# Performance work log

Measured on AMD Instinct MI355X. Metric: run time of the kernel, lower is better.

The kernel has to match this reference:

```python
import jax, jax.numpy as jnp
import numpy as np

B, C = 2048, 512          # batch, channels
CHG = 16                  # coarse grid side (16x16 -> N=256)
FHG = 16                  # fine grid side (16x16 -> F=256)
N = CHG * CHG             # coarse_span.total
F = FHG * FHG             # fine_total
K = 4                     # top4 sample mode
LOG_F = float(np.log(F))


def _ln(x, g, b, eps=1e-5):
    m = jnp.mean(x, axis=-1, keepdims=True)
    v = jnp.var(x, axis=-1, keepdims=True)
    return (x - m) * jax.lax.rsqrt(v + eps) * g + b


def _mlp3(x, w1, b1, w2, b2, w3, b3):
    # linear_stack: Linear+gelu, Linear+gelu, Linear (dropout=0 / eval)
    h = jax.nn.gelu(x @ w1 + b1)
    h = jax.nn.gelu(h @ w2 + b2)
    return h @ w3 + b3


def setup_inputs() -> dict:
    key = jax.random.key(0)
    ks = jax.random.split(key, 10)
    s = 0.02
    return {
        'x': jax.random.normal(ks[0], (B, C), jnp.float32),
        'in_g': jnp.ones((C,), jnp.float32), 'in_b': jnp.zeros((C,), jnp.float32),
        'nop_w': jax.random.normal(ks[1], (C, 1), jnp.float32) * s,
        'nop_b': jnp.zeros((1,), jnp.float32),
        'c_w1': jax.random.normal(ks[2], (C, C), jnp.float32) * s,
        'c_b1': jnp.zeros((C,), jnp.float32),
        'c_w2': jax.random.normal(ks[3], (C, C), jnp.float32) * s,
        'c_b2': jnp.zeros((C,), jnp.float32),
        'c_w3': jax.random.normal(ks[4], (C, N), jnp.float32) * s,
        'c_b3': jnp.zeros((N,), jnp.float32),
        'emb': jax.random.normal(ks[5], (N, C), jnp.float32),
        'emb_g': jnp.ones((C,), jnp.float32), 'emb_b': jnp.zeros((C,), jnp.float32),
        'f_w1': jax.random.normal(ks[6], (2 * C, C), jnp.float32) * s,
        'f_b1': jnp.zeros((C,), jnp.float32),
        'f_w2': jax.random.normal(ks[7], (C, C), jnp.float32) * s,
        'f_b2': jnp.zeros((C,), jnp.float32),
        'f_w3': jax.random.normal(ks[8], (C, F), jnp.float32) * s,
        'f_b3': jnp.zeros((F,), jnp.float32),
    }


def reference(x, in_g, in_b, nop_w, nop_b, c_w1, c_b1, c_w2, c_b2, c_w3, c_b3,
              emb, emb_g, emb_b, f_w1, f_b1, f_w2, f_b2, f_w3, f_b3):
    xn = _ln(x, in_g, in_b)                                  # (B,C)
    no_op = xn @ nop_w + nop_b                               # (B,1)
    coarse = _mlp3(xn, c_w1, c_b1, c_w2, c_b2, c_w3, c_b3)   # (B,N)
    _, idx = jax.lax.top_k(coarse, K)                        # (B,K) int32
    e = _ln(emb[idx], emb_g, emb_b)                          # (B,K,C)
    fin = jnp.concatenate([jnp.broadcast_to(xn[:, None, :], (B, K, C)), e], axis=-1)
    fine = _mlp3(fin, f_w1, f_b1, f_w2, f_b2, f_w3, f_b3)    # (B,K,F)
    # scatter value: coarse[b,i] - log F + fine + log F - lse(fine) = coarse[b,i] + log_softmax(fine)
    vals = jnp.take_along_axis(coarse, idx, axis=1)[:, :, None] + jax.nn.log_softmax(fine, axis=-1)
    dense = jnp.broadcast_to((coarse - LOG_F)[:, :, None], (B, N, F))
    dense = dense.at[jnp.arange(B)[:, None], idx].set(vals)  # top-k indices are distinct
    # view (B, ch0, ch1, fh0, fh1) -> permute (0,1,3,2,4) -> flatten
    xname = dense.reshape(B, CHG, CHG, FHG, FHG).transpose(0, 1, 3, 2, 4).reshape(B, -1)
    return jnp.concatenate([no_op, xname], axis=-1)          # (B, 1 + N*F)
```

## Files before the change

kernel.cpp:

```cpp
#include <hip/hip_runtime.h>
#include <math.h>

#define BATCH 2048
#define CH 512
#define N_COARSE 256
#define F_FINE 256
#define K_TOP 4
#define OUT_STRIDE 65537

typedef unsigned short ushort_t;
typedef __bf16 bf16x8 __attribute__((ext_vector_type(8)));
typedef float f32x4 __attribute__((ext_vector_type(4)));

__device__ __forceinline__ float gelu_tanh(float x) {
    float x3 = x * x * x;
    float t = tanhf(0.7978845608028654f * (x + 0.044715f * x3));
    return 0.5f * x * (1.0f + t);
}

__device__ __forceinline__ ushort_t f2bf(float f) {
    unsigned u = __float_as_uint(f);
    unsigned r = (u + 0x7FFF + ((u >> 16) & 1)) >> 16;
    return (ushort_t)r;
}
__device__ __forceinline__ float bf2f(ushort_t h) {
    return __uint_as_float(((unsigned)h) << 16);
}

__global__ __launch_bounds__(256) void prep_kernel(
    const float* __restrict__ f_w1, const float* __restrict__ f_w2, const float* __restrict__ f_w3,
    ushort_t* __restrict__ wt1, ushort_t* __restrict__ wt2, ushort_t* __restrict__ wt3,
    const float* __restrict__ c_w1, const float* __restrict__ c_w2, const float* __restrict__ c_w3,
    ushort_t* __restrict__ cwt1, ushort_t* __restrict__ cwt2, ushort_t* __restrict__ cwt3,
    const float* __restrict__ x, const float* __restrict__ g, const float* __restrict__ b,
    const float* __restrict__ nop_w, const float* __restrict__ nop_b,
    ushort_t* __restrict__ xnsp, float* __restrict__ out)
{
    __shared__ float s[32][33];
    int blk = blockIdx.x;
    int t = threadIdx.x;
    if (blk < 1536) {
        const float* W; ushort_t* Wt; int Kd, Nd, gx, gy; bool split;
        if (blk < 512)       { W=f_w1; Wt=wt1; Kd=1024; Nd=512; gx=blk&15; gy=blk>>4; split=false; }
        else if (blk < 768)  { int u=blk-512;  W=f_w2; Wt=wt2; Kd=512; Nd=512; gx=u&15; gy=u>>4; split=false; }
        else if (blk < 896)  { int u=blk-768;  W=f_w3; Wt=wt3; Kd=512; Nd=256; gx=u&7;  gy=u>>3; split=false; }
        else if (blk < 1152) { int u=blk-896;  W=c_w1; Wt=cwt1; Kd=512; Nd=512; gx=u&15; gy=u>>4; split=true; }
        else if (blk < 1408) { int u=blk-1152; W=c_w2; Wt=cwt2; Kd=512; Nd=512; gx=u&15; gy=u>>4; split=true; }
        else                 { int u=blk-1408; W=c_w3; Wt=cwt3; Kd=512; Nd=256; gx=u&7;  gy=u>>3; split=true; }
        int tx = t & 31, ty = t >> 5;
        int n0 = gx * 32, k0 = gy * 32;
        #pragma unroll
        for (int i = 0; i < 4; ++i) {
            int r = ty + i * 8;
            s[r][tx] = W[(size_t)(k0 + r) * Nd + n0 + tx];
        }
        __syncthreads();
        if (!split) {
            #pragma unroll
            for (int i = 0; i < 4; ++i) {
                int r = ty + i * 8;
                Wt[(size_t)(n0 + r) * Kd + k0 + tx] = f2bf(s[tx][r]);
            }
        } else {
            #pragma unroll
            for (int i = 0; i < 4; ++i) {
                int r = ty + i * 8;
                float v = s[tx][r];
                ushort_t h = f2bf(v);
                Wt[(size_t)(n0 + r) * 1024 + k0 + tx] = h;
                Wt[(size_t)(n0 + r) * 1024 + 512 + k0 + tx] = f2bf(v - bf2f(h));
            }
        }
    } else {
        float* red = &s[0][0];
        int row = blk - 1536;
        int lane = t & 63, wave = t >> 6;
        const float* xr = x + (size_t)row * CH;
        float v0 = xr[t], v1 = xr[t + 256];
        float sm = v0 + v1, ss = v0 * v0 + v1 * v1;
        #pragma unroll
        for (int off = 32; off; off >>= 1) { sm += __shfl_xor(sm, off); ss += __shfl_xor(ss, off); }
        if (lane == 0) { red[wave] = sm; red[4 + wave] = ss; }
        __syncthreads();
        sm = red[0] + red[1] + red[2] + red[3];
        ss = red[4] + red[5] + red[6] + red[7];
        float mean = sm * (1.0f / CH);
        float var = ss * (1.0f / CH) - mean * mean;
        float rsq = rsqrtf(var + 1e-5f);
        float xn0 = (v0 - mean) * rsq * g[t] + b[t];
        float xn1 = (v1 - mean) * rsq * g[t + 256] + b[t + 256];
        ushort_t* xr2 = xnsp + (size_t)row * 1024;
        ushort_t h0 = f2bf(xn0), h1v = f2bf(xn1);
        xr2[t] = h0; xr2[t + 256] = h1v;
        xr2[512 + t] = f2bf(xn0 - bf2f(h0));
        xr2[512 + t + 256] = f2bf(xn1 - bf2f(h1v));
        float d = xn0 * nop_w[t] + xn1 * nop_w[t + 256];
        #pragma unroll
        for (int off = 32; off; off >>= 1) d += __shfl_xor(d, off);
        __syncthreads();
        if (lane == 0) red[wave] = d;
        __syncthreads();
        if (t == 0) out[(size_t)row * OUT_STRIDE] = red[0] + red[1] + red[2] + red[3] + nop_b[0];
    }
}

template<int MODE, int MT, int NT, int OUTM>
__global__ __launch_bounds__(256) void mfma_gemm_kernel(
    const ushort_t* __restrict__ A1, const ushort_t* __restrict__ A2,
    const ushort_t* __restrict__ Wt, const float* __restrict__ bias,
    const float* __restrict__ cvals, void* __restrict__ Cout, int Nd, int Ktot)
{
    constexpr int AI = MT / 64, BI = NT / 64;
    constexpr int FI = MT / 32, FJ = NT / 32;
    __shared__ ushort_t As[2][MT * 32];
    __shared__ ushort_t Bs[2][NT * 32];
    __shared__ float mxs[64 * 2];
    __shared__ float ses[64 * 2];
    int t = threadIdx.x;
    int n0 = blockIdx.x * NT, m0 = blockIdx.y * MT;
    int wave = t >> 6, lane = t & 63;
    int wm = (wave & 1) * (MT / 2), wn = (wave >> 1) * (NT / 2);
    int lr = lane & 15, quad = lane >> 4;

    f32x4 acc[FI][FJ] = {};
    float4 aReg[AI], bReg[BI];

    auto loadAB = [&](int k0) {
        int aoff = (MODE == 2) ? ((k0 >= 1024) ? k0 - 512 : (k0 & 511)) : k0;
        int woff = (MODE == 2) ? ((k0 >= 1024) ? k0 - 1024 : k0) : k0;
        #pragma unroll
        for (int i = 0; i < AI; ++i) {
            int c = i * 256 + t, r = c >> 2, q = (c & 3) * 8;
            int gr = m0 + r;
            const ushort_t* ap;
            if (MODE == 1)      ap = (k0 < 512) ? A1 + (size_t)(gr >> 2) * 1024 + k0 + q
                                                : A2 + (size_t)gr * 512 + (k0 - 512) + q;
            else if (MODE == 2) ap = A1 + (size_t)gr * 1024 + aoff + q;
            else                ap = A1 + (size_t)gr * Ktot + k0 + q;
            aReg[i] = *(const float4*)ap;
        }
        #pragma unroll
        for (int i = 0; i < BI; ++i) {
            int c = i * 256 + t, r = c >> 2, q = (c & 3) * 8;
            size_t wstride = (MODE == 2) ? 1024 : (size_t)Ktot;
            bReg[i] = *(const float4*)(Wt + (size_t)(n0 + r) * wstride + woff + q);
        }
    };
    auto storeAB = [&](int p) {
        #pragma unroll
        for (int i = 0; i < AI; ++i) { int c = i * 256 + t; *(float4*)&As[p][c * 8] = aReg[i]; }
        #pragma unroll
        for (int i = 0; i < BI; ++i) { int c = i * 256 + t; *(float4*)&Bs[p][c * 8] = bReg[i]; }
    };

    loadAB(0);
    storeAB(0);
    int steps = Ktot >> 5;
    int p = 0;
    for (int s = 0; s < steps; ++s) {
        __syncthreads();
        if (s + 1 < steps) loadAB((s + 1) * 32);
        bf16x8 af[FI], bfr[FJ];
        #pragma unroll
        for (int i = 0; i < FI; ++i)
            af[i] = *(const bf16x8*)&As[p][(wm + i * 16 + lr) * 32 + quad * 8];
        #pragma unroll
        for (int j = 0; j < FJ; ++j)
            bfr[j] = *(const bf16x8*)&Bs[p][(wn + j * 16 + lr) * 32 + quad * 8];
        #pragma unroll
        for (int i = 0; i < FI; ++i)
            #pragma unroll
            for (int j = 0; j < FJ; ++j)
                acc[i][j] = __builtin_amdgcn_mfma_f32_16x16x32_bf16(af[i], bfr[j], acc[i][j], 0, 0, 0);
        if (s + 1 < steps) storeAB(p ^ 1);
        p ^= 1;
    }

    if (OUTM == 3) {
        float bv[FJ];
        #pragma unroll
        for (int j = 0; j < FJ; ++j) bv[j] = bias[wn + j * 16 + lr];
        int half = wave >> 1;
        float rmx[FI][4];
        #pragma unroll
        for (int i = 0; i < FI; ++i)
            #pragma unroll
            for (int r = 0; r < 4; ++r) {
                float m = -1e30f;
                #pragma unroll
                for (int j = 0; j < FJ; ++j) m = fmaxf(m, acc[i][j][r] + bv[j]);
                #pragma unroll
                for (int mk = 1; mk < 16; mk <<= 1) m = fmaxf(m, __shfl_xor(m, mk));
                if (lr == 0) mxs[(wm + i * 16 + quad * 4 + r) * 2 + half] = m;
            }
        __syncthreads();
        #pragma unroll
        for (int i = 0; i < FI; ++i)
            #pragma unroll
            for (int r = 0; r < 4; ++r) {
                int rl = wm + i * 16 + quad * 4 + r;
                rmx[i][r] = fmaxf(mxs[rl * 2], mxs[rl * 2 + 1]);
            }
        #pragma unroll
        for (int i = 0; i < FI; ++i)
            #pragma unroll
            for (int r = 0; r < 4; ++r) {
                float sv = 0.f;
                #pragma unroll
                for (int j = 0; j < FJ; ++j) sv += expf(acc[i][j][r] + bv[j] - rmx[i][r]);
                #pragma unroll
                for (int mk = 1; mk < 16; mk <<= 1) sv += __shfl_xor(sv, mk);
                if (lr == 0) ses[(wm + i * 16 + quad * 4 + r) * 2 + half] = sv;
            }
        __syncthreads();
        float* outp = (float*)Cout;
        #pragma unroll
        for (int i = 0; i < FI; ++i)
            #pragma unroll
            for (int r = 0; r < 4; ++r) {
                int rl = wm + i * 16 + quad * 4 + r;
                float se = ses[rl * 2] + ses[rl * 2 + 1];
                float addc = cvals[m0 + rl] - rmx[i][r] - logf(se);
                #pragma unroll
                for (int j = 0; j < FJ; ++j)
                    outp[(size_t)(m0 + rl) * Nd + wn + j * 16 + lr] = acc[i][j][r] + bv[j] + addc;
            }
    } else {
        #pragma unroll
        for (int j = 0; j < FJ; ++j) {
            int col = n0 + wn + j * 16 + lr;
            float bvv = bias[col];
            #pragma unroll
            for (int i = 0; i < FI; ++i) {
                #pragma unroll
                for (int r = 0; r < 4; ++r) {
                    int row = m0 + wm + i * 16 + quad * 4 + r;
                    float val = acc[i][j][r] + bvv;
                    if (OUTM == 0) {
                        ((ushort_t*)Cout)[(size_t)row * Nd + col] = f2bf(gelu_tanh(val));
                    } else if (OUTM == 1) {
                        float gv = gelu_tanh(val);
                        ushort_t h = f2bf(gv);
                        ((ushort_t*)Cout)[(size_t)row * 1024 + col] = h;
                        ((ushort_t*)Cout)[(size_t)row * 1024 + 512 + col] = f2bf(gv - bf2f(h));
                    } else {
                        ((float*)Cout)[(size_t)row * Nd + col] = val;
                    }
                }
            }
        }
    }
}

__global__ __launch_bounds__(256) void topk_embln_kernel(
    const float* __restrict__ coarse, const float* __restrict__ emb,
    const float* __restrict__ g, const float* __restrict__ b,
    int* __restrict__ idx, float* __restrict__ cvals, ushort_t* __restrict__ e_bf)
{
    int brow = blockIdx.x;
    int t = threadIdx.x;
    int wave = t >> 6, lane = t & 63;
    __shared__ int sidx[4];

    if (wave == 0) {
        const float* cr = coarse + (size_t)brow * N_COARSE;
        float v[4]; int id[4];
        #pragma unroll
        for (int j = 0; j < 4; ++j) { v[j] = cr[lane + 64 * j]; id[j] = lane + 64 * j; }
        #pragma unroll
        for (int r = 0; r < K_TOP; ++r) {
            float bv = v[0]; int bi = id[0];
            #pragma unroll
            for (int j = 1; j < 4; ++j)
                if (v[j] > bv || (v[j] == bv && id[j] < bi)) { bv = v[j]; bi = id[j]; }
            #pragma unroll
            for (int off = 32; off; off >>= 1) {
                float ov = __shfl_xor(bv, off); int oi = __shfl_xor(bi, off);
                if (ov > bv || (ov == bv && oi < bi)) { bv = ov; bi = oi; }
            }
            if ((bi & 63) == lane) v[bi >> 6] = -INFINITY;
            if (lane == 0) {
                sidx[r] = bi;
                idx[brow * K_TOP + r] = bi;
                cvals[brow * K_TOP + r] = bv;
            }
        }
    }
    __syncthreads();

    int n = sidx[wave];
    const float* er = emb + (size_t)n * CH + lane * 8;
    float4 u0 = *(const float4*)er;
    float4 u1 = *(const float4*)(er + 4);
    float s  = u0.x + u0.y + u0.z + u0.w + u1.x + u1.y + u1.z + u1.w;
    float ss = u0.x * u0.x + u0.y * u0.y + u0.z * u0.z + u0.w * u0.w
             + u1.x * u1.x + u1.y * u1.y + u1.z * u1.z + u1.w * u1.w;
    #pragma unroll
    for (int off = 32; off; off >>= 1) { s += __shfl_xor(s, off); ss += __shfl_xor(ss, off); }
    float mean = s * (1.0f / CH);
    float var = ss * (1.0f / CH) - mean * mean;
    float rsq = rsqrtf(var + 1e-5f);
    float4 g0 = *(const float4*)(g + lane * 8), g1 = *(const float4*)(g + lane * 8 + 4);
    float4 b0 = *(const float4*)(b + lane * 8), b1 = *(const float4*)(b + lane * 8 + 4);
    uint4 pk;
    pk.x = (unsigned)f2bf((u0.x - mean) * rsq * g0.x + b0.x) |
           ((unsigned)f2bf((u0.y - mean) * rsq * g0.y + b0.y) << 16);
    pk.y = (unsigned)f2bf((u0.z - mean) * rsq * g0.z + b0.z) |
           ((unsigned)f2bf((u0.w - mean) * rsq * g0.w + b0.w) << 16);
    pk.z = (unsigned)f2bf((u1.x - mean) * rsq * g1.x + b1.x) |
           ((unsigned)f2bf((u1.y - mean) * rsq * g1.y + b1.y) << 16);
    pk.w = (unsigned)f2bf((u1.z - mean) * rsq * g1.z + b1.z) |
           ((unsigned)f2bf((u1.w - mean) * rsq * g1.w + b1.w) << 16);
    *(uint4*)(e_bf + (size_t)(brow * K_TOP + wave) * CH + lane * 8) = pk;
}

__global__ __launch_bounds__(256) void scatter_kernel(
    const float* __restrict__ coarse, const float* __restrict__ fine,
    const int* __restrict__ idx, float* __restrict__ out)
{
    const float LOG_F = 5.545177444479562f;
    int b = blockIdx.y;
    __shared__ int sidx[4];
    if (threadIdx.x < 4) sidx[threadIdx.x] = idx[b * 4 + threadIdx.x];
    __syncthreads();
    int i0 = sidx[0], i1 = sidx[1], i2 = sidx[2], i3 = sidx[3];
    size_t rowb = (size_t)b * OUT_STRIDE + 1;
    #pragma unroll
    for (int q = 0; q < 4; ++q) {
        int o = blockIdx.x * 4096 + q * 1024 + threadIdx.x * 4;
        int c0 = o >> 12, f0 = (o >> 8) & 15, c1 = (o >> 4) & 15, f1 = o & 15;
        int n = c0 * 16 + c1;
        int f = f0 * 16 + f1;
        int k = -1;
        if (n == i0) k = 0; else if (n == i1) k = 1; else if (n == i2) k = 2; else if (n == i3) k = 3;
        float r0, r1, r2, r3;
        if (k >= 0) {
            float4 u = *(const float4*)(fine + ((size_t)(b * 4 + k)) * F_FINE + f);
            r0 = u.x; r1 = u.y; r2 = u.z; r3 = u.w;
        } else {
            float base = coarse[(size_t)b * N_COARSE + n] - LOG_F;
            r0 = r1 = r2 = r3 = base;
        }
        float* p = out + rowb + o;
        __builtin_nontemporal_store(r0, p + 0);
        __builtin_nontemporal_store(r1, p + 1);
        __builtin_nontemporal_store(r2, p + 2);
        __builtin_nontemporal_store(r3, p + 3);
    }
}

extern "C" void kernel_launch(void* const* d_in, const int* in_sizes, int n_in,
                              void* d_out, int out_size, void* d_ws, size_t ws_size,
                              hipStream_t stream) {
    const float* x     = (const float*)d_in[0];
    const float* in_g  = (const float*)d_in[1];
    const float* in_b  = (const float*)d_in[2];
    const float* nop_w = (const float*)d_in[3];
    const float* nop_b = (const float*)d_in[4];
    const float* c_w1  = (const float*)d_in[5];
    const float* c_b1  = (const float*)d_in[6];
    const float* c_w2  = (const float*)d_in[7];
    const float* c_b2  = (const float*)d_in[8];
    const float* c_w3  = (const float*)d_in[9];
    const float* c_b3  = (const float*)d_in[10];
    const float* emb   = (const float*)d_in[11];
    const float* emb_g = (const float*)d_in[12];
    const float* emb_b = (const float*)d_in[13];
    const float* f_w1  = (const float*)d_in[14];
    const float* f_b1  = (const float*)d_in[15];
    const float* f_w2  = (const float*)d_in[16];
    const float* f_b2  = (const float*)d_in[17];
    const float* f_w3  = (const float*)d_in[18];
    const float* f_b3  = (const float*)d_in[19];

    float* ws = (float*)d_ws;
    float* coarse  = ws;
    float* fine    = coarse + 524288;
    ushort_t* xnsp   = (ushort_t*)(fine + 2097152);
    ushort_t* h1sp   = xnsp + 2097152;
    ushort_t* h2sp   = h1sp + 2097152;
    ushort_t* e_bf   = h2sp + 2097152;
    ushort_t* fh1_bf = e_bf + 4194304;
    ushort_t* fh2_bf = fh1_bf + 4194304;
    ushort_t* wt1    = fh2_bf + 4194304;
    ushort_t* wt2    = wt1 + 524288;
    ushort_t* wt3    = wt2 + 262144;
    ushort_t* cwt1   = wt3 + 131072;
    ushort_t* cwt2   = cwt1 + 524288;
    ushort_t* cwt3   = cwt2 + 524288;
    int*   idxb   = (int*)(cwt3 + 262144);
    float* cvals  = (float*)(idxb + 8192);

    float* out = (float*)d_out;

    prep_kernel<<<3584, 256, 0, stream>>>(
        f_w1, f_w2, f_w3, wt1, wt2, wt3,
        c_w1, c_w2, c_w3, cwt1, cwt2, cwt3,
        x, in_g, in_b, nop_w, nop_b, xnsp, out);
    mfma_gemm_kernel<2, 64, 64, 1><<<dim3(8, 32), 256, 0, stream>>>(
        xnsp, nullptr, cwt1, c_b1, nullptr, h1sp, 512, 1536);
    mfma_gemm_kernel<2, 64, 64, 1><<<dim3(8, 32), 256, 0, stream>>>(
        h1sp, nullptr, cwt2, c_b2, nullptr, h2sp, 512, 1536);
    mfma_gemm_kernel<2, 64, 64, 2><<<dim3(4, 32), 256, 0, stream>>>(
        h2sp, nullptr, cwt3, c_b3, nullptr, coarse, 256, 1536);
    topk_embln_kernel<<<BATCH, 256, 0, stream>>>(coarse, emb, emb_g, emb_b, idxb, cvals, e_bf);
    mfma_gemm_kernel<1, 64, 128, 0><<<dim3(4, 128), 256, 0, stream>>>(
        xnsp, e_bf, wt1, f_b1, nullptr, fh1_bf, 512, 1024);
    mfma_gemm_kernel<0, 64, 128, 0><<<dim3(4, 128), 256, 0, stream>>>(
        fh1_bf, nullptr, wt2, f_b2, nullptr, fh2_bf, 512, 512);
    mfma_gemm_kernel<0, 64, 256, 3><<<dim3(1, 128), 256, 0, stream>>>(
        fh2_bf, nullptr, wt3, f_b3, cvals, fine, 256, 512);
    scatter_kernel<<<dim3(16, BATCH), 256, 0, stream>>>(coarse, fine, idxb, out);
}
```

Baseline: 760.2 us.

## Fuse all stages into one persistent cooperative kernel with grid syncs

Replaces the sequence of nine kernel launches with a single cooperative persistent kernel of 256 blocks that runs each stage in a loop over work units and separates stages with grid-wide barriers. The fine-MLP GEMMs use larger 128x128 tiles to fit the fixed grid. This targets launch gaps and tail effects between small stages, but limits the bandwidth-bound scatter and other stages to one block per CU, which may reduce memory-level parallelism. A fallback to the original multi-kernel path is kept if the cooperative launch fails.

```diff
diff --git a/kernel.cpp b/kernel.cpp
--- a/kernel.cpp
+++ b/kernel.cpp
@@ -1,5 +1,8 @@
 #include <hip/hip_runtime.h>
+#include <hip/hip_cooperative_groups.h>
 #include <math.h>
+
+namespace cg = cooperative_groups;
 
 #define BATCH 2048
 #define CH 512
@@ -27,26 +30,27 @@
     return __uint_as_float(((unsigned)h) << 16);
 }
 
-__global__ __launch_bounds__(256) void prep_kernel(
-    const float* __restrict__ f_w1, const float* __restrict__ f_w2, const float* __restrict__ f_w3,
-    ushort_t* __restrict__ wt1, ushort_t* __restrict__ wt2, ushort_t* __restrict__ wt3,
-    const float* __restrict__ c_w1, const float* __restrict__ c_w2, const float* __restrict__ c_w3,
-    ushort_t* __restrict__ cwt1, ushort_t* __restrict__ cwt2, ushort_t* __restrict__ cwt3,
-    const float* __restrict__ x, const float* __restrict__ g, const float* __restrict__ b,
-    const float* __restrict__ nop_w, const float* __restrict__ nop_b,
-    ushort_t* __restrict__ xnsp, float* __restrict__ out)
-{
-    __shared__ float s[32][33];
-    int blk = blockIdx.x;
-    int t = threadIdx.x;
-    if (blk < 1536) {
+struct Params {
+    const float *x, *in_g, *in_b, *nop_w, *nop_b;
+    const float *c_w1, *c_b1, *c_w2, *c_b2, *c_w3, *c_b3;
+    const float *emb, *emb_g, *emb_b;
+    const float *f_w1, *f_b1, *f_w2, *f_b2, *f_w3, *f_b3;
+    float *coarse, *fine, *out, *cvals;
+    ushort_t *xnsp, *h1sp, *h2sp, *e_bf, *fh1_bf, *fh2_bf;
+    ushort_t *wt1, *wt2, *wt3, *cwt1, *cwt2, *cwt3;
+    int *idxb;
+};
+
+__device__ __forceinline__ void prep_unit(char* smem, int u, int t, const Params& p) {
+    if (u < 1536) {
+        float (*s)[33] = (float(*)[33])smem;
         const float* W; ushort_t* Wt; int Kd, Nd, gx, gy; bool split;
-        if (blk < 512)       { W=f_w1; Wt=wt1; Kd=1024; Nd=512; gx=blk&15; gy=blk>>4; split=false; }
-        else if (blk < 768)  { int u=blk-512;  W=f_w2; Wt=wt2; Kd=512; Nd=512; gx=u&15; gy=u>>4; split=false; }
-        else if (blk < 896)  { int u=blk-768;  W=f_w3; Wt=wt3; Kd=512; Nd=256; gx=u&7;  gy=u>>3; split=false; }
-        else if (blk < 1152) { int u=blk-896;  W=c_w1; Wt=cwt1; Kd=512; Nd=512; gx=u&15; gy=u>>4; split=true; }
-        else if (blk < 1408) { int u=blk-1152; W=c_w2; Wt=cwt2; Kd=512; Nd=512; gx=u&15; gy=u>>4; split=true; }
-        else                 { int u=blk-1408; W=c_w3; Wt=cwt3; Kd=512; Nd=256; gx=u&7;  gy=u>>3; split=true; }
+        if (u < 512)       { W=p.f_w1; Wt=p.wt1; Kd=1024; Nd=512; gx=u&15; gy=u>>4; split=false; }
+        else if (u < 768)  { int v=u-512;  W=p.f_w2; Wt=p.wt2; Kd=512; Nd=512; gx=v&15; gy=v>>4; split=false; }
+        else if (u < 896)  { int v=u-768;  W=p.f_w3; Wt=p.wt3; Kd=512; Nd=256; gx=v&7;  gy=v>>3; split=false; }
+        else if (u < 1152) { int v=u-896;  W=p.c_w1; Wt=p.cwt1; Kd=512; Nd=512; gx=v&15; gy=v>>4; split=true; }
+        else if (u < 1408) { int v=u-1152; W=p.c_w2; Wt=p.cwt2; Kd=512; Nd=512; gx=v&15; gy=v>>4; split=true; }
+        else               { int v=u-1408; W=p.c_w3; Wt=p.cwt3; Kd=512; Nd=256; gx=v&7;  gy=v>>3; split=true; }
         int tx = t & 31, ty = t >> 5;
         int n0 = gx * 32, k0 = gy * 32;
         #pragma unroll
@@ -72,10 +76,10 @@
             }
         }
     } else {
-        float* red = &s[0][0];
-        int row = blk - 1536;
+        float* red = (float*)smem;
+        int row = u - 1536;
         int lane = t & 63, wave = t >> 6;
-        const float* xr = x + (size_t)row * CH;
+        const float* xr = p.x + (size_t)row * CH;
         float v0 = xr[t], v1 = xr[t + 256];
         float sm = v0 + v1, ss = v0 * v0 + v1 * v1;
         #pragma unroll
@@ -87,37 +91,36 @@
         float mean = sm * (1.0f / CH);
         float var = ss * (1.0f / CH) - mean * mean;
         float rsq = rsqrtf(var + 1e-5f);
-        float xn0 = (v0 - mean) * rsq * g[t] + b[t];
-        float xn1 = (v1 - mean) * rsq * g[t + 256] + b[t + 256];
-        ushort_t* xr2 = xnsp + (size_t)row * 1024;
+        float xn0 = (v0 - mean) * rsq * p.in_g[t] + p.in_b[t];
+        float xn1 = (v1 - mean) * rsq * p.in_g[t + 256] + p.in_b[t + 256];
+        ushort_t* xr2 = p.xnsp + (size_t)row * 1024;
         ushort_t h0 = f2bf(xn0), h1v = f2bf(xn1);
         xr2[t] = h0; xr2[t + 256] = h1v;
         xr2[512 + t] = f2bf(xn0 - bf2f(h0));
         xr2[512 + t + 256] = f2bf(xn1 - bf2f(h1v));
-        float d = xn0 * nop_w[t] + xn1 * nop_w[t + 256];
+        float d = xn0 * p.nop_w[t] + xn1 * p.nop_w[t + 256];
         #pragma unroll
         for (int off = 32; off; off >>= 1) d += __shfl_xor(d, off);
         __syncthreads();
         if (lane == 0) red[wave] = d;
         __syncthreads();
-        if (t == 0) out[(size_t)row * OUT_STRIDE] = red[0] + red[1] + red[2] + red[3] + nop_b[0];
+        if (t == 0) p.out[(size_t)row * OUT_STRIDE] = red[0] + red[1] + red[2] + red[3] + p.nop_b[0];
     }
 }
 
 template<int MODE, int MT, int NT, int OUTM>
-__global__ __launch_bounds__(256) void mfma_gemm_kernel(
+__device__ __forceinline__ void mfma_tile(
+    char* smem, int t, int n0, int m0,
     const ushort_t* __restrict__ A1, const ushort_t* __restrict__ A2,
     const ushort_t* __restrict__ Wt, const float* __restrict__ bias,
     const float* __restrict__ cvals, void* __restrict__ Cout, int Nd, int Ktot)
 {
     constexpr int AI = MT / 64, BI = NT / 64;
     constexpr int FI = MT / 32, FJ = NT / 32;
-    __shared__ ushort_t As[2][MT * 32];
-    __shared__ ushort_t Bs[2][NT * 32];
-    __shared__ float mxs[64 * 2];
-    __shared__ float ses[64 * 2];
-    int t = threadIdx.x;
-    int n0 = blockIdx.x * NT, m0 = blockIdx.y * MT;
+    ushort_t* As = (ushort_t*)smem;
+    ushort_t* Bs = (ushort_t*)(smem + MT * 128);
+    float* mxs = (float*)(smem + (MT + NT) * 128);
+    float* ses = mxs + 128;
     int wave = t >> 6, lane = t & 63;
     int wm = (wave & 1) * (MT / 2), wn = (wave >> 1) * (NT / 2);
     int lr = lane & 15, quad = lane >> 4;
@@ -148,9 +151,9 @@
     };
     auto storeAB = [&](int p) {
         #pragma unroll
-        for (int i = 0; i < AI; ++i) { int c = i * 256 + t; *(float4*)&As[p][c * 8] = aReg[i]; }
-        #pragma unroll
-        for (int i = 0; i < BI; ++i) { int c = i * 256 + t; *(float4*)&Bs[p][c * 8] = bReg[i]; }
+        for (int i = 0; i < AI; ++i) { int c = i * 256 + t; *(float4*)&As[p * MT * 32 + c * 8] = aReg[i]; }
+        #pragma unroll
+        for (int i = 0; i < BI; ++i) { int c = i * 256 + t; *(float4*)&Bs[p * NT * 32 + c * 8] = bReg[i]; }
     };
 
     loadAB(0);
@@ -163,10 +166,10 @@
         bf16x8 af[FI], bfr[FJ];
         #pragma unroll
         for (int i = 0; i < FI; ++i)
-            af[i] = *(const bf16x8*)&As[p][(wm + i * 16 + lr) * 32 + quad * 8];
+            af[i] = *(const bf16x8*)&As[p * MT * 32 + (wm + i * 16 + lr) * 32 + quad * 8];
         #pragma unroll
         for (int j = 0; j < FJ; ++j)
-            bfr[j] = *(const bf16x8*)&Bs[p][(wn + j * 16 + lr) * 32 + quad * 8];
+            bfr[j] = *(const bf16x8*)&Bs[p * NT * 32 + (wn + j * 16 + lr) * 32 + quad * 8];
         #pragma unroll
         for (int i = 0; i < FI; ++i)
             #pragma unroll
@@ -252,18 +255,11 @@
     }
 }
 
-__global__ __launch_bounds__(256) void topk_embln_kernel(
-    const float* __restrict__ coarse, const float* __restrict__ emb,
-    const float* __restrict__ g, const float* __restrict__ b,
-    int* __restrict__ idx, float* __restrict__ cvals, ushort_t* __restrict__ e_bf)
-{
-    int brow = blockIdx.x;
-    int t = threadIdx.x;
+__device__ __forceinline__ void topk_embln_block(char* smem, int brow, int t, const Params& p) {
     int wave = t >> 6, lane = t & 63;
-    __shared__ int sidx[4];
-
+    int* sidx = (int*)smem;
     if (wave == 0) {
-        const float* cr = coarse + (size_t)brow * N_COARSE;
+        const float* cr = p.coarse + (size_t)brow * N_COARSE;
         float v[4]; int id[4];
         #pragma unroll
         for (int j = 0; j < 4; ++j) { v[j] = cr[lane + 64 * j]; id[j] = lane + 64 * j; }
@@ -281,15 +277,14 @@
             if ((bi & 63) == lane) v[bi >> 6] = -INFINITY;
             if (lane == 0) {
                 sidx[r] = bi;
-                idx[brow * K_TOP + r] = bi;
-                cvals[brow * K_TOP + r] = bv;
+                p.idxb[brow * K_TOP + r] = bi;
+                p.cvals[brow * K_TOP + r] = bv;
             }
         }
     }
     __syncthreads();
-
     int n = sidx[wave];
-    const float* er = emb + (size_t)n * CH + lane * 8;
+    const float* er = p.emb + (size_t)n * CH + lane * 8;
     float4 u0 = *(const float4*)er;
     float4 u1 = *(const float4*)(er + 4);
     float s  = u0.x + u0.y + u0.z + u0.w + u1.x + u1.y + u1.z + u1.w;
@@ -300,8 +295,8 @@
     float mean = s * (1.0f / CH);
     float var = ss * (1.0f / CH) - mean * mean;
     float rsq = rsqrtf(var + 1e-5f);
-    float4 g0 = *(const float4*)(g + lane * 8), g1 = *(const float4*)(g + lane * 8 + 4);
-    float4 b0 = *(const float4*)(b + lane * 8), b1 = *(const float4*)(b + lane * 8 + 4);
+    float4 g0 = *(const float4*)(p.emb_g + lane * 8), g1 = *(const float4*)(p.emb_g + lane * 8 + 4);
+    float4 b0 = *(const float4*)(p.emb_b + lane * 8), b1 = *(const float4*)(p.emb_b + lane * 8 + 4);
     uint4 pk;
     pk.x = (unsigned)f2bf((u0.x - mean) * rsq * g0.x + b0.x) |
            ((unsigned)f2bf((u0.y - mean) * rsq * g0.y + b0.y) << 16);
@@ -311,104 +306,158 @@
            ((unsigned)f2bf((u1.y - mean) * rsq * g1.y + b1.y) << 16);
     pk.w = (unsigned)f2bf((u1.z - mean) * rsq * g1.z + b1.z) |
            ((unsigned)f2bf((u1.w - mean) * rsq * g1.w + b1.w) << 16);
-    *(uint4*)(e_bf + (size_t)(brow * K_TOP + wave) * CH + lane * 8) = pk;
-}
-
-__global__ __launch_bounds__(256) void scatter_kernel(
-    const float* __restrict__ coarse, const float* __restrict__ fine,
-    const int* __restrict__ idx, float* __restrict__ out)
-{
+    *(uint4*)(p.e_bf + (size_t)(brow * K_TOP + wave) * CH + lane * 8) = pk;
+}
+
+__device__ __forceinline__ void scatter_unit(int b, int cx, int t, const Params& p) {
     const float LOG_F = 5.545177444479562f;
-    int b = blockIdx.y;
-    __shared__ int sidx[4];
-    if (threadIdx.x < 4) sidx[threadIdx.x] = idx[b * 4 + threadIdx.x];
-    __syncthreads();
-    int i0 = sidx[0], i1 = sidx[1], i2 = sidx[2], i3 = sidx[3];
+    int4 ii = *(const int4*)&p.idxb[b * 4];
     size_t rowb = (size_t)b * OUT_STRIDE + 1;
     #pragma unroll
     for (int q = 0; q < 4; ++q) {
-        int o = blockIdx.x * 4096 + q * 1024 + threadIdx.x * 4;
+        int o = cx * 4096 + q * 1024 + t * 4;
         int c0 = o >> 12, f0 = (o >> 8) & 15, c1 = (o >> 4) & 15, f1 = o & 15;
         int n = c0 * 16 + c1;
         int f = f0 * 16 + f1;
         int k = -1;
-        if (n == i0) k = 0; else if (n == i1) k = 1; else if (n == i2) k = 2; else if (n == i3) k = 3;
+        if (n == ii.x) k = 0; else if (n == ii.y) k = 1; else if (n == ii.z) k = 2; else if (n == ii.w) k = 3;
         float r0, r1, r2, r3;
         if (k >= 0) {
-            float4 u = *(const float4*)(fine + ((size_t)(b * 4 + k)) * F_FINE + f);
+            float4 u = *(const float4*)(p.fine + ((size_t)(b * 4 + k)) * F_FINE + f);
             r0 = u.x; r1 = u.y; r2 = u.z; r3 = u.w;
         } else {
-            float base = coarse[(size_t)b * N_COARSE + n] - LOG_F;
+            float base = p.coarse[(size_t)b * N_COARSE + n] - LOG_F;
             r0 = r1 = r2 = r3 = base;
         }
-        float* p = out + rowb + o;
-        __builtin_nontemporal_store(r0, p + 0);
-        __builtin_nontemporal_store(r1, p + 1);
-        __builtin_nontemporal_store(r2, p + 2);
-        __builtin_nontemporal_store(r3, p + 3);
-    }
+        float* op = p.out + rowb + o;
+        __builtin_nontemporal_store(r0, op + 0);
+        __builtin_nontemporal_store(r1, op + 1);
+        __builtin_nontemporal_store(r2, op + 2);
+        __builtin_nontemporal_store(r3, op + 3);
+    }
+}
+
+__global__ void mega_kernel(Params p) {
+    __shared__ __attribute__((aligned(16))) char smem[41984];
+    cg::grid_group grid = cg::this_grid();
+    int blk = blockIdx.x, t = threadIdx.x;
+
+    for (int u = blk; u < 3584; u += 256) { prep_unit(smem, u, t, p); __syncthreads(); }
+    grid.sync();
+    mfma_tile<2, 64, 64, 1>(smem, t, (blk & 7) * 64, (blk >> 3) * 64,
+                            p.xnsp, nullptr, p.cwt1, p.c_b1, nullptr, p.h1sp, 512, 1536);
+    grid.sync();
+    mfma_tile<2, 64, 64, 1>(smem, t, (blk & 7) * 64, (blk >> 3) * 64,
+                            p.h1sp, nullptr, p.cwt2, p.c_b2, nullptr, p.h2sp, 512, 1536);
+    grid.sync();
+    if (blk < 128)
+        mfma_tile<2, 64, 64, 2>(smem, t, (blk & 3) * 64, (blk >> 2) * 64,
+                                p.h2sp, nullptr, p.cwt3, p.c_b3, nullptr, p.coarse, 256, 1536);
+    grid.sync();
+    for (int it = 0; it < 8; ++it) { topk_embln_block(smem, blk + it * 256, t, p); __syncthreads(); }
+    grid.sync();
+    mfma_tile<1, 128, 128, 0>(smem, t, (blk & 3) * 128, (blk >> 2) * 128,
+                              p.xnsp, p.e_bf, p.wt1, p.f_b1, nullptr, p.fh1_bf, 512, 1024);
+    grid.sync();
+    mfma_tile<0, 128, 128, 0>(smem, t, (blk & 3) * 128, (blk >> 2) * 128,
+                              p.fh1_bf, nullptr, p.wt2, p.f_b2, nullptr, p.fh2_bf, 512, 512);
+    grid.sync();
+    if (blk < 128)
+        mfma_tile<0, 64, 256, 3>(smem, t, 0, blk * 64,
+                                 p.fh2_bf, nullptr, p.wt3, p.f_b3, p.cvals, p.fine, 256, 512);
+    grid.sync();
+    for (int it = 0; it < 128; ++it) { int u = blk + it * 256; scatter_unit(u >> 4, u & 15, t, p); }
+}
+
+__global__ __launch_bounds__(256) void prep_kernel(Params p) {
+    __shared__ __attribute__((aligned(16))) char smem[4224];
+    prep_unit(smem, blockIdx.x, threadIdx.x, p);
+}
+
+template<int MODE, int MT, int NT, int OUTM>
+__global__ __launch_bounds__(256) void mfma_gemm_kernel(
+    const ushort_t* __restrict__ A1, const ushort_t* __restrict__ A2,
+    const ushort_t* __restrict__ Wt, const float* __restrict__ bias,
+    const float* __restrict__ cvals, void* __restrict__ Cout, int Nd, int Ktot)
+{
+    constexpr int SB = (MT + NT) * 128 + (OUTM == 3 ? 1024 : 0);
+    __shared__ __attribute__((aligned(16))) char smem[SB];
+    mfma_tile<MODE, MT, NT, OUTM>(smem, threadIdx.x, blockIdx.x * NT, blockIdx.y * MT,
+                                  A1, A2, Wt, bias, cvals, Cout, Nd, Ktot);
+}
+
+__global__ __launch_bounds__(256) void topk_embln_kernel(Params p) {
+    __shared__ __attribute__((aligned(16))) char smem[16];
+    topk_embln_block(smem, blockIdx.x, threadIdx.x, p);
+}
+
+__global__ __launch_bounds__(256) void scatter_kernel(Params p) {
+    scatter_unit(blockIdx.y, blockIdx.x, threadIdx.x, p);
 }
 
 extern "C" void kernel_launch(void* const* d_in, const int* in_sizes, int n_in,
                               void* d_out, int out_size, void* d_ws, size_t ws_size,
                               hipStream_t stream) {
-    const float* x     = (const float*)d_in[0];
-    const float* in_g  = (const float*)d_in[1];
-    const float* in_b  = (const float*)d_in[2];
-    const float* nop_w = (const float*)d_in[3];
-    const float* nop_b = (const float*)d_in[4];
-    const float* c_w1  = (const float*)d_in[5];
-    const float* c_b1  = (const float*)d_in[6];
-    const float* c_w2  = (const float*)d_in[7];
-    const float* c_b2  = (const float*)d_in[8];
-    const float* c_w3  = (const float*)d_in[9];
-    const float* c_b3  = (const float*)d_in[10];
-    const float* emb   = (const float*)d_in[11];
-    const float* emb_g = (const float*)d_in[12];
-    const float* emb_b = (const float*)d_in[13];
-    const float* f_w1  = (const float*)d_in[14];
-    const float* f_b1  = (const float*)d_in[15];
-    const float* f_w2  = (const float*)d_in[16];
-    const float* f_b2  = (const float*)d_in[17];
-    const float* f_w3  = (const float*)d_in[18];
-    const float* f_b3  = (const float*)d_in[19];
+    Params prm;
+    prm.x     = (const float*)d_in[0];
+    prm.in_g  = (const float*)d_in[1];
+    prm.in_b  = (const float*)d_in[2];
+    prm.nop_w = (const float*)d_in[3];
+    prm.nop_b = (const float*)d_in[4];
+    prm.c_w1  = (const float*)d_in[5];
+    prm.c_b1  = (const float*)d_in[6];
+    prm.c_w2  = (const float*)d_in[7];
+    prm.c_b2  = (const float*)d_in[8];
+    prm.c_w3  = (const float*)d_in[9];
+    prm.c_b3  = (const float*)d_in[10];
+    prm.emb   = (const float*)d_in[11];
+    prm.emb_g = (const float*)d_in[12];
+    prm.emb_b = (const float*)d_in[13];
+    prm.f_w1  = (const float*)d_in[14];
+    prm.f_b1  = (const float*)d_in[15];
+    prm.f_w2  = (const float*)d_in[16];
+    prm.f_b2  = (const float*)d_in[17];
+    prm.f_w3  = (const float*)d_in[18];
+    prm.f_b3  = (const float*)d_in[19];
 
     float* ws = (float*)d_ws;
-    float* coarse  = ws;
-    float* fine    = coarse + 524288;
-    ushort_t* xnsp   = (ushort_t*)(fine + 2097152);
-    ushort_t* h1sp   = xnsp + 2097152;
-    ushort_t* h2sp   = h1sp + 2097152;
-    ushort_t* e_bf   = h2sp + 2097152;
-    ushort_t* fh1_bf = e_bf + 4194304;
-    ushort_t* fh2_bf = fh1_bf + 4194304;
-    ushort_t* wt1    = fh2_bf + 4194304;
-    ushort_t* wt2    = wt1 + 524288;
-    ushort_t* wt3    = wt2 + 262144;
-    ushort_t* cwt1   = wt3 + 131072;
-    ushort_t* cwt2   = cwt1 + 524288;
-    ushort_t* cwt3   = cwt2 + 524288;
-    int*   idxb   = (int*)(cwt3 + 262144);
-    float* cvals  = (float*)(idxb + 8192);
-
-    float* out = (float*)d_out;
-
-    prep_kernel<<<3584, 256, 0, stream>>>(
-        f_w1, f_w2, f_w3, wt1, wt2, wt3,
-        c_w1, c_w2, c_w3, cwt1, cwt2, cwt3,
-        x, in_g, in_b, nop_w, nop_b, xnsp, out);
-    mfma_gemm_kernel<2, 64, 64, 1><<<dim3(8, 32), 256, 0, stream>>>(
-        xnsp, nullptr, cwt1, c_b1, nullptr, h1sp, 512, 1536);
-    mfma_gemm_kernel<2, 64, 64, 1><<<dim3(8, 32), 256, 0, stream>>>(
-        h1sp, nullptr, cwt2, c_b2, nullptr, h2sp, 512, 1536);
-    mfma_gemm_kernel<2, 64, 64, 2><<<dim3(4, 32), 256, 0, stream>>>(
-        h2sp, nullptr, cwt3, c_b3, nullptr, coarse, 256, 1536);
-    topk_embln_kernel<<<BATCH, 256, 0, stream>>>(coarse, emb, emb_g, emb_b, idxb, cvals, e_bf);
-    mfma_gemm_kernel<1, 64, 128, 0><<<dim3(4, 128), 256, 0, stream>>>(
-        xnsp, e_bf, wt1, f_b1, nullptr, fh1_bf, 512, 1024);
-    mfma_gemm_kernel<0, 64, 128, 0><<<dim3(4, 128), 256, 0, stream>>>(
-        fh1_bf, nullptr, wt2, f_b2, nullptr, fh2_bf, 512, 512);
-    mfma_gemm_kernel<0, 64, 256, 3><<<dim3(1, 128), 256, 0, stream>>>(
-        fh2_bf, nullptr, wt3, f_b3, cvals, fine, 256, 512);
-    scatter_kernel<<<dim3(16, BATCH), 256, 0, stream>>>(coarse, fine, idxb, out);
-}
+    prm.coarse  = ws;
+    prm.fine    = prm.coarse + 524288;
+    prm.xnsp    = (ushort_t*)(prm.fine + 2097152);
+    prm.h1sp    = prm.xnsp + 2097152;
+    prm.h2sp    = prm.h1sp + 2097152;
+    prm.e_bf    = prm.h2sp + 2097152;
+    prm.fh1_bf  = prm.e_bf + 4194304;
+    prm.fh2_bf  = prm.fh1_bf + 4194304;
+    prm.wt1     = prm.fh2_bf + 4194304;
+    prm.wt2     = prm.wt1 + 524288;
+    prm.wt3     = prm.wt2 + 262144;
+    prm.cwt1    = prm.wt3 + 131072;
+    prm.cwt2    = prm.cwt1 + 524288;
+    prm.cwt3    = prm.cwt2 + 524288;
+    prm.idxb    = (int*)(prm.cwt3 + 262144);
+    prm.cvals   = (float*)(prm.idxb + 8192);
+    prm.out     = (float*)d_out;
+
+    void* kargs[] = { (void*)&prm };
+    hipError_t err = hipLaunchCooperativeKernel((const void*)mega_kernel, dim3(256), dim3(256),
+                                                kargs, 0, stream);
+    if (err != hipSuccess) {
+        (void)hipGetLastError();
+        prep_kernel<<<3584, 256, 0, stream>>>(prm);
+        mfma_gemm_kernel<2, 64, 64, 1><<<dim3(8, 32), 256, 0, stream>>>(
+            prm.xnsp, nullptr, prm.cwt1, prm.c_b1, nullptr, prm.h1sp, 512, 1536);
+        mfma_gemm_kernel<2, 64, 64, 1><<<dim3(8, 32), 256, 0, stream>>>(
+            prm.h1sp, nullptr, prm.cwt2, prm.c_b2, nullptr, prm.h2sp, 512, 1536);
+        mfma_gemm_kernel<2, 64, 64, 2><<<dim3(4, 32), 256, 0, stream>>>(
+            prm.h2sp, nullptr, prm.cwt3, prm.c_b3, nullptr, prm.coarse, 256, 1536);
+        topk_embln_kernel<<<BATCH, 256, 0, stream>>>(prm);
+        mfma_gemm_kernel<1, 64, 128, 0><<<dim3(4, 128), 256, 0, stream>>>(
+            prm.xnsp, prm.e_bf, prm.wt1, prm.f_b1, nullptr, prm.fh1_bf, 512, 1024);
+        mfma_gemm_kernel<0, 64, 128, 0><<<dim3(4, 128), 256, 0, stream>>>(
+            prm.fh1_bf, nullptr, prm.wt2, prm.f_b2, nullptr, prm.fh2_bf, 512, 512);
+        mfma_gemm_kernel<0, 64, 256, 3><<<dim3(1, 128), 256, 0, stream>>>(
+            prm.fh2_bf, nullptr, prm.wt3, prm.f_b3, prm.cvals, prm.fine, 256, 512);
+        scatter_kernel<<<dim3(16, BATCH), 256, 0, stream>>>(prm);
+    }
+}
```

Measured after the change: 1.080 ms. +42.0%, slower.
